# Optimization experiments

Measured on AMD Instinct MI355X. Metric: run time of the kernel, lower is better.

Reference implementation:

```python
import jax, jax.numpy as jnp
import numpy as np

D_IN, D_HID, D_OUT, N_EXP, N_TOK = 1024, 4096, 1024, 8, 4096


def setup_inputs() -> dict:
    key = jax.random.key(0)
    ks = jax.random.split(key, 7)
    x = jax.random.normal(ks[0], (N_TOK, D_IN), dtype=jnp.float32)
    s1 = 1.0 / np.sqrt(D_IN).astype(np.float32)
    s2 = 1.0 / np.sqrt(D_HID).astype(np.float32)
    W1 = jax.random.uniform(ks[1], (N_EXP, D_IN, D_HID), jnp.float32, -s1, s1)
    b1 = jax.random.uniform(ks[2], (N_EXP, D_HID), jnp.float32, -s1, s1)
    W2 = jax.random.uniform(ks[3], (N_EXP, D_HID, D_OUT), jnp.float32, -s2, s2)
    b2 = jax.random.uniform(ks[4], (N_EXP, D_OUT), jnp.float32, -s2, s2)
    Wg = jax.random.uniform(ks[5], (D_IN, N_EXP), jnp.float32, -s1, s1)
    bg = jax.random.uniform(ks[6], (N_EXP,), jnp.float32, -s1, s1)
    return {"x": x, "W1": W1, "b1": b1, "W2": W2, "b2": b2,
            "Wg": Wg, "bg": bg, "top_k": 2}


def reference(x, W1, b1, W2, b2, Wg, bg, top_k):
    # Gating: softmax over experts, then top-k and renormalizing softmax.
    gates = jax.nn.softmax(x @ Wg + bg, axis=-1)            # [N, E]
    topk_vals, topk_idx = jax.lax.top_k(gates, top_k)       # [N, k]
    topk_w = jax.nn.softmax(topk_vals, axis=-1)             # [N, k]
    # Dense all-expert MLP (vectorized replacement for per-token Python loop).
    h = jax.nn.relu(jnp.einsum('nd,edh->neh', x, W1) + b1)  # [N, E, H]
    y = jnp.einsum('neh,eho->neo', h, W2) + b2              # [N, E, O]
    # Combine: gather each token's top-k expert outputs, weighted sum.
    sel = jnp.take_along_axis(y, topk_idx[:, :, None], axis=1)  # [N, k, O]
    out = jnp.sum(topk_w[:, :, None] * sel, axis=1)             # [N, O]
    return out
```

## Files before the change

kernel.cpp:

```cpp
#include <hip/hip_runtime.h>
#include <hip/hip_bf16.h>

#define NTOK 4096
#define DIN  1024
#define DHID 4096
#define DOUT 1024
#define NEXP 8
#define TMAX 72

typedef __hip_bfloat16 bf16;
typedef short short8 __attribute__((ext_vector_type(8)));
typedef short short4v __attribute__((ext_vector_type(4)));
typedef float floatx4 __attribute__((ext_vector_type(4)));

#define WAIT_VM0 0x0F70
#define WAIT_VM4 0x0F74

#define WS_XB    0ull
#define WS_W1T   8388608ull
#define WS_W2T   75497472ull
#define WS_H     142606336ull
#define WS_META  209715200ull
#define MO_CNT    0
#define MO_OFF    64
#define MO_TILE_E 128
#define MO_TILE_S 512
#define MO_TILE_R 896
#define MO_NT     1280
#define MO_CURG   1344
#define MO_T2I    1536
#define MO_T2W    34304
#define MO_ROWS   67072
#define MO_ROWW   99840

__device__ __forceinline__ void gload16(const bf16* g, bf16* l) {
  __builtin_amdgcn_global_load_lds(
      (const __attribute__((address_space(1))) void*)g,
      (__attribute__((address_space(3))) void*)l, 16, 0, 0);
}

__global__ void k_transpose_cast(const float* __restrict__ in, bf16* __restrict__ out,
                                 int R, int C) {
  __shared__ float t[64][65];
  size_t ebase = (size_t)blockIdx.z * R * C;
  int c0 = blockIdx.x * 64, r0 = blockIdx.y * 64;
  int tid = threadIdx.x;
  int rr = tid >> 4;
  int cq = (tid & 15) * 4;
  #pragma unroll
  for (int i = 0; i < 4; i++) {
    int r = rr + i * 16;
    float4 v = *(const float4*)(in + ebase + (size_t)(r0 + r) * C + c0 + cq);
    t[cq + 0][r] = v.x; t[cq + 1][r] = v.y; t[cq + 2][r] = v.z; t[cq + 3][r] = v.w;
  }
  __syncthreads();
  int cc = tid >> 3;
  int rq = (tid & 7) * 8;
  #pragma unroll
  for (int i = 0; i < 2; i++) {
    int c = cc + i * 32;
    union { int4 v; bf16 h[8]; } u;
    #pragma unroll
    for (int j = 0; j < 8; j++) u.h[j] = __float2bfloat16(t[c][rq + j]);
    *(int4*)(out + ebase + (size_t)(c0 + c) * R + r0 + rq) = u.v;
  }
}

__global__ void k_gate(const float* __restrict__ x, const float* __restrict__ Wg,
                       const float* __restrict__ bg, bf16* __restrict__ xb,
                       int* __restrict__ t2i, float* __restrict__ t2w,
                       int* __restrict__ cnt) {
  int wave = threadIdx.x >> 6, lane = threadIdx.x & 63;
  int t = blockIdx.x * 4 + wave;
  const float* xr = x + (size_t)t * DIN;
  bf16* xbr = xb + (size_t)t * DIN;
  float acc[8] = {0.f, 0.f, 0.f, 0.f, 0.f, 0.f, 0.f, 0.f};
  #pragma unroll
  for (int i = 0; i < 4; i++) {
    int d0 = (lane + i * 64) * 4;
    float4 v = *(const float4*)(xr + d0);
    union { short4v s; bf16 h[4]; } u;
    u.h[0] = __float2bfloat16(v.x); u.h[1] = __float2bfloat16(v.y);
    u.h[2] = __float2bfloat16(v.z); u.h[3] = __float2bfloat16(v.w);
    *(short4v*)(xbr + d0) = u.s;
    float xv4[4] = {v.x, v.y, v.z, v.w};
    #pragma unroll
    for (int c = 0; c < 4; c++) {
      const float* wr = Wg + (size_t)(d0 + c) * 8;
      float4 w0 = *(const float4*)wr;
      float4 w1 = *(const float4*)(wr + 4);
      float xv = xv4[c];
      acc[0] += xv * w0.x; acc[1] += xv * w0.y; acc[2] += xv * w0.z; acc[3] += xv * w0.w;
      acc[4] += xv * w1.x; acc[5] += xv * w1.y; acc[6] += xv * w1.z; acc[7] += xv * w1.w;
    }
  }
  #pragma unroll
  for (int off = 32; off; off >>= 1) {
    #pragma unroll
    for (int e = 0; e < 8; e++) acc[e] += __shfl_xor(acc[e], off, 64);
  }
  if (lane == 0) {
    float p[8], m = -1e30f, s = 0.f;
    #pragma unroll
    for (int e = 0; e < 8; e++) { p[e] = acc[e] + bg[e]; m = fmaxf(m, p[e]); }
    #pragma unroll
    for (int e = 0; e < 8; e++) { p[e] = expf(p[e] - m); s += p[e]; }
    float inv = 1.f / s;
    #pragma unroll
    for (int e = 0; e < 8; e++) p[e] *= inv;
    int i0 = 0;
    #pragma unroll
    for (int e = 1; e < 8; e++) if (p[e] > p[i0]) i0 = e;
    int i1 = (i0 == 0) ? 1 : 0;
    #pragma unroll
    for (int e = 0; e < 8; e++) if (e != i0 && p[e] > p[i1]) i1 = e;
    float d = expf(p[i1] - p[i0]);
    float w0 = 1.f / (1.f + d), w1 = d / (1.f + d);
    t2i[2 * t] = i0; t2i[2 * t + 1] = i1;
    t2w[2 * t] = w0; t2w[2 * t + 1] = w1;
    atomicAdd(&cnt[i0], 1);
    atomicAdd(&cnt[i1], 1);
  }
}

__global__ void k_meta(const int* __restrict__ cnt, int* __restrict__ off,
                       int* __restrict__ tile_e, int* __restrict__ tile_s,
                       int* __restrict__ tile_r, int* __restrict__ nt,
                       int* __restrict__ cur_g) {
  if (threadIdx.x == 0) {
    int o = 0, n = 0;
    for (int e = 0; e < 8; e++) {
      off[e] = o; cur_g[e] = o;
      int c = cnt[e];
      for (int r = 0; r < c; r += 128) {
        tile_e[n] = e; tile_s[n] = o + r; tile_r[n] = min(128, c - r); n++;
      }
      o += c;
    }
    *nt = n;
  }
}

__global__ void k_scatter(const int* __restrict__ t2i, const float* __restrict__ t2w,
                          int* __restrict__ cur_g, int* __restrict__ rows,
                          float* __restrict__ roww) {
  __shared__ int lcnt[8], lbase[8];
  if (threadIdx.x < 8) lcnt[threadIdx.x] = 0;
  __syncthreads();
  int t = blockIdx.x * 256 + threadIdx.x;
  int e0 = t2i[2 * t], e1 = t2i[2 * t + 1];
  int p0 = atomicAdd(&lcnt[e0], 1);
  int p1 = atomicAdd(&lcnt[e1], 1);
  __syncthreads();
  if (threadIdx.x < 8)
    lbase[threadIdx.x] = atomicAdd(&cur_g[threadIdx.x], lcnt[threadIdx.x]);
  __syncthreads();
  int a0 = lbase[e0] + p0, a1 = lbase[e1] + p1;
  rows[a0] = t; roww[a0] = t2w[2 * t];
  rows[a1] = t; roww[a1] = t2w[2 * t + 1];
}

template <int MODE>
__global__ __launch_bounds__(256)
void k_gemm(const bf16* __restrict__ A, const bf16* __restrict__ Bt,
            const float* __restrict__ bias,
            const int* __restrict__ tile_e, const int* __restrict__ tile_s,
            const int* __restrict__ tile_r, const int* __restrict__ nt,
            const int* __restrict__ rows, const float* __restrict__ roww,
            bf16* __restrict__ hout, float* __restrict__ out,
            int K, int N) {
  int hwid = blockIdx.x + blockIdx.y * gridDim.x;
  int xcd = hwid & 7, pos = hwid >> 3;
  int tile = xcd * 9 + pos % 9;
  if (tile >= *nt) return;
  int n0 = (pos / 9) * 128;
  int e = tile_e[tile], start = tile_s[tile], mrows = tile_r[tile];
  int tid = threadIdx.x, lane = tid & 63, wave = tid >> 6;
  int wm = wave & 1, wn = wave >> 1;

  __shared__ bf16 Al[3][128 * 32];
  __shared__ bf16 Bl[3][128 * 32];

  int srow = tid >> 2;
  int rot = (srow >> 1) & 3;
  int kc8 = (((tid & 3) - rot) & 3) * 8;
  int ra0 = srow, ra1 = 64 + srow;
  int er0 = ra0 < mrows ? ra0 : 0;
  int er1 = ra1 < mrows ? ra1 : 0;
  size_t ga0, ga1;
  if (MODE == 1) {
    ga0 = (size_t)rows[start + er0] * K;
    ga1 = (size_t)rows[start + er1] * K;
  } else {
    ga0 = (size_t)(start + er0) * K;
    ga1 = (size_t)(start + er1) * K;
  }
  const bf16* ap0 = A + ga0 + kc8;
  const bf16* ap1 = A + ga1 + kc8;
  const bf16* bb = Bt + (size_t)e * K * N + (size_t)n0 * K;
  const bf16* bp0 = bb + (size_t)srow * K + kc8;
  const bf16* bp1 = bb + (size_t)(64 + srow) * K + kc8;

  floatx4 zz = {0.f, 0.f, 0.f, 0.f};
  floatx4 acc[4][4];
  #pragma unroll
  for (int i = 0; i < 4; i++)
    #pragma unroll
    for (int j = 0; j < 4; j++) acc[i][j] = zz;

  int fr = lane & 15;
  int ko = (((lane >> 4) + ((fr >> 1) & 3)) & 3) * 8;

#define STAGE(buf, kk)                                    \
  do {                                                    \
    gload16(ap0 + (kk), &Al[buf][tid * 8]);               \
    gload16(ap1 + (kk), &Al[buf][2048 + tid * 8]);        \
    gload16(bp0 + (kk), &Bl[buf][tid * 8]);               \
    gload16(bp1 + (kk), &Bl[buf][2048 + tid * 8]);        \
  } while (0)

  STAGE(0, 0);
  STAGE(1, 32);

  int nk = K >> 5;
  int cur = 0;
  for (int t = 0; t < nk; ++t) {
    if (t + 1 < nk) __builtin_amdgcn_s_waitcnt(WAIT_VM4);
    else            __builtin_amdgcn_s_waitcnt(WAIT_VM0);
    __builtin_amdgcn_s_barrier();

    short8 af[4], bfr[4];
    #pragma unroll
    for (int i = 0; i < 4; i++)
      af[i] = *(const short8*)&Al[cur][(wm * 64 + i * 16 + fr) * 32 + ko];
    #pragma unroll
    for (int j = 0; j < 4; j++)
      bfr[j] = *(const short8*)&Bl[cur][(wn * 64 + j * 16 + fr) * 32 + ko];

    if (t + 2 < nk) {
      int nb = cur + 2; if (nb >= 3) nb -= 3;
      STAGE(nb, (t + 2) * 32);
    }

    #pragma unroll
    for (int i = 0; i < 4; i++)
      #pragma unroll
      for (int j = 0; j < 4; j++)
        acc[i][j] = __builtin_amdgcn_mfma_f32_16x16x32_bf16(af[i], bfr[j], acc[i][j], 0, 0, 0);
    cur = (cur + 1 == 3) ? 0 : cur + 1;
  }
#undef STAGE

  int col_l = lane & 15, quad = lane >> 4;
  if (MODE == 1) {
    #pragma unroll
    for (int i = 0; i < 4; i++) {
      #pragma unroll
      for (int r = 0; r < 4; r++) {
        int row = wm * 64 + i * 16 + quad * 4 + r;
        if (row < mrows) {
          size_t rb = (size_t)(start + row) * N;
          #pragma unroll
          for (int j = 0; j < 4; j++) {
            int col = n0 + wn * 64 + j * 16 + col_l;
            float v = acc[i][j][r] + bias[e * N + col];
            hout[rb + col] = __float2bfloat16(fmaxf(v, 0.f));
          }
        }
      }
    }
  } else {
    #pragma unroll
    for (int i = 0; i < 4; i++) {
      #pragma unroll
      for (int r = 0; r < 4; r++) {
        int row = wm * 64 + i * 16 + quad * 4 + r;
        if (row < mrows) {
          int tok = rows[start + row];
          float w = roww[start + row];
          size_t ob = (size_t)tok * N;
          #pragma unroll
          for (int j = 0; j < 4; j++) {
            int col = n0 + wn * 64 + j * 16 + col_l;
            float v = (acc[i][j][r] + bias[e * N + col]) * w;
            unsafeAtomicAdd(&out[ob + col], v);
          }
        }
      }
    }
  }
}

extern "C" void kernel_launch(void* const* d_in, const int* in_sizes, int n_in,
                              void* d_out, int out_size, void* d_ws, size_t ws_size,
                              hipStream_t stream) {
  const float* x  = (const float*)d_in[0];
  const float* W1 = (const float*)d_in[1];
  const float* b1 = (const float*)d_in[2];
  const float* W2 = (const float*)d_in[3];
  const float* b2 = (const float*)d_in[4];
  const float* Wg = (const float*)d_in[5];
  const float* bg = (const float*)d_in[6];
  float* out = (float*)d_out;
  char* ws = (char*)d_ws;

  bf16* xb  = (bf16*)(ws + WS_XB);
  bf16* w1t = (bf16*)(ws + WS_W1T);
  bf16* w2t = (bf16*)(ws + WS_W2T);
  bf16* h   = (bf16*)(ws + WS_H);
  char* meta = ws + WS_META;
  int*   cnt    = (int*)(meta + MO_CNT);
  int*   off    = (int*)(meta + MO_OFF);
  int*   tile_e = (int*)(meta + MO_TILE_E);
  int*   tile_s = (int*)(meta + MO_TILE_S);
  int*   tile_r = (int*)(meta + MO_TILE_R);
  int*   nt     = (int*)(meta + MO_NT);
  int*   cur_g  = (int*)(meta + MO_CURG);
  int*   t2i    = (int*)(meta + MO_T2I);
  float* t2w    = (float*)(meta + MO_T2W);
  int*   rows   = (int*)(meta + MO_ROWS);
  float* roww   = (float*)(meta + MO_ROWW);

  hipMemsetAsync(cnt, 0, 64, stream);
  hipMemsetAsync(d_out, 0, (size_t)out_size * sizeof(float), stream);

  k_transpose_cast<<<dim3(DHID / 64, DIN / 64, NEXP), 256, 0, stream>>>(W1, w1t, DIN, DHID);
  k_transpose_cast<<<dim3(DOUT / 64, DHID / 64, NEXP), 256, 0, stream>>>(W2, w2t, DHID, DOUT);
  k_gate<<<NTOK / 4, 256, 0, stream>>>(x, Wg, bg, xb, t2i, t2w, cnt);
  k_meta<<<1, 64, 0, stream>>>(cnt, off, tile_e, tile_s, tile_r, nt, cur_g);
  k_scatter<<<NTOK / 256, 256, 0, stream>>>(t2i, t2w, cur_g, rows, roww);
  k_gemm<1><<<dim3(TMAX, DHID / 128), 256, 0, stream>>>(
      xb, w1t, b1, tile_e, tile_s, tile_r, nt, rows, roww, h, nullptr, DIN, DHID);
  k_gemm<2><<<dim3(TMAX, DOUT / 128), 256, 0, stream>>>(
      h, w2t, b2, tile_e, tile_s, tile_r, nt, rows, roww, nullptr, out, DHID, DOUT);
}
```

Before: 672.3 us.

## Widen grouped GEMM tile to 128x256 and parallelize tile metadata build

The expert GEMM tile doubles in N from 128 to 256, so each wave computes 64x128 with 32 accumulators. B staging grows to four loads per stage and the wait count is adjusted to match. This gives more MFMA work per A-fragment load and halves the grid, at the cost of higher register pressure (launch bounds now ask for 2 blocks) and fewer blocks to fill the CUs. The serial single-thread k_meta loop is also replaced by a parallel per-thread tile assignment.

Result: slower. 694.3 us (+3.3%).

```diff
diff --git a/kernel.cpp b/kernel.cpp
--- a/kernel.cpp
+++ b/kernel.cpp
@@ -14,7 +14,7 @@
 typedef float floatx4 __attribute__((ext_vector_type(4)));
 
 #define WAIT_VM0 0x0F70
-#define WAIT_VM4 0x0F74
+#define WAIT_VM6 0x0F76
 
 #define WS_XB    0ull
 #define WS_W1T   8388608ull
@@ -127,17 +127,22 @@
                        int* __restrict__ tile_e, int* __restrict__ tile_s,
                        int* __restrict__ tile_r, int* __restrict__ nt,
                        int* __restrict__ cur_g) {
-  if (threadIdx.x == 0) {
-    int o = 0, n = 0;
-    for (int e = 0; e < 8; e++) {
-      off[e] = o; cur_g[e] = o;
-      int c = cnt[e];
-      for (int r = 0; r < c; r += 128) {
-        tile_e[n] = e; tile_s[n] = o + r; tile_r[n] = min(128, c - r); n++;
-      }
-      o += c;
-    }
-    *nt = n;
+  int t = threadIdx.x;
+  int c[8], o[8], tb[8];
+  int acc = 0, tacc = 0;
+  #pragma unroll
+  for (int e = 0; e < 8; e++) {
+    c[e] = cnt[e]; o[e] = acc; acc += c[e];
+    tb[e] = tacc; tacc += (c[e] + 127) >> 7;
+  }
+  if (t < 8) { off[t] = o[t]; cur_g[t] = o[t]; }
+  if (t == 0) *nt = tacc;
+  if (t < tacc) {
+    int e = 0;
+    #pragma unroll
+    for (int k = 1; k < 8; k++) if (t >= tb[k]) e = k;
+    int r = (t - tb[e]) << 7;
+    tile_e[t] = e; tile_s[t] = o[e] + r; tile_r[t] = min(128, c[e] - r);
   }
 }
 
@@ -161,7 +166,7 @@
 }
 
 template <int MODE>
-__global__ __launch_bounds__(256)
+__global__ __launch_bounds__(256, 2)
 void k_gemm(const bf16* __restrict__ A, const bf16* __restrict__ Bt,
             const float* __restrict__ bias,
             const int* __restrict__ tile_e, const int* __restrict__ tile_s,
@@ -173,13 +178,13 @@
   int xcd = hwid & 7, pos = hwid >> 3;
   int tile = xcd * 9 + pos % 9;
   if (tile >= *nt) return;
-  int n0 = (pos / 9) * 128;
+  int n0 = (pos / 9) * 256;
   int e = tile_e[tile], start = tile_s[tile], mrows = tile_r[tile];
   int tid = threadIdx.x, lane = tid & 63, wave = tid >> 6;
   int wm = wave & 1, wn = wave >> 1;
 
   __shared__ bf16 Al[3][128 * 32];
-  __shared__ bf16 Bl[3][128 * 32];
+  __shared__ bf16 Bl[3][256 * 32];
 
   int srow = tid >> 2;
   int rot = (srow >> 1) & 3;
@@ -200,13 +205,15 @@
   const bf16* bb = Bt + (size_t)e * K * N + (size_t)n0 * K;
   const bf16* bp0 = bb + (size_t)srow * K + kc8;
   const bf16* bp1 = bb + (size_t)(64 + srow) * K + kc8;
+  const bf16* bp2 = bb + (size_t)(128 + srow) * K + kc8;
+  const bf16* bp3 = bb + (size_t)(192 + srow) * K + kc8;
 
   floatx4 zz = {0.f, 0.f, 0.f, 0.f};
-  floatx4 acc[4][4];
+  floatx4 acc[4][8];
   #pragma unroll
   for (int i = 0; i < 4; i++)
     #pragma unroll
-    for (int j = 0; j < 4; j++) acc[i][j] = zz;
+    for (int j = 0; j < 8; j++) acc[i][j] = zz;
 
   int fr = lane & 15;
   int ko = (((lane >> 4) + ((fr >> 1) & 3)) & 3) * 8;
@@ -217,6 +224,8 @@
     gload16(ap1 + (kk), &Al[buf][2048 + tid * 8]);        \
     gload16(bp0 + (kk), &Bl[buf][tid * 8]);               \
     gload16(bp1 + (kk), &Bl[buf][2048 + tid * 8]);        \
+    gload16(bp2 + (kk), &Bl[buf][4096 + tid * 8]);        \
+    gload16(bp3 + (kk), &Bl[buf][6144 + tid * 8]);        \
   } while (0)
 
   STAGE(0, 0);
@@ -225,17 +234,17 @@
   int nk = K >> 5;
   int cur = 0;
   for (int t = 0; t < nk; ++t) {
-    if (t + 1 < nk) __builtin_amdgcn_s_waitcnt(WAIT_VM4);
+    if (t + 1 < nk) __builtin_amdgcn_s_waitcnt(WAIT_VM6);
     else            __builtin_amdgcn_s_waitcnt(WAIT_VM0);
     __builtin_amdgcn_s_barrier();
 
-    short8 af[4], bfr[4];
+    short8 af[4], bfr[8];
     #pragma unroll
     for (int i = 0; i < 4; i++)
       af[i] = *(const short8*)&Al[cur][(wm * 64 + i * 16 + fr) * 32 + ko];
     #pragma unroll
-    for (int j = 0; j < 4; j++)
-      bfr[j] = *(const short8*)&Bl[cur][(wn * 64 + j * 16 + fr) * 32 + ko];
+    for (int j = 0; j < 8; j++)
+      bfr[j] = *(const short8*)&Bl[cur][(wn * 128 + j * 16 + fr) * 32 + ko];
 
     if (t + 2 < nk) {
       int nb = cur + 2; if (nb >= 3) nb -= 3;
@@ -245,7 +254,7 @@
     #pragma unroll
     for (int i = 0; i < 4; i++)
       #pragma unroll
-      for (int j = 0; j < 4; j++)
+      for (int j = 0; j < 8; j++)
         acc[i][j] = __builtin_amdgcn_mfma_f32_16x16x32_bf16(af[i], bfr[j], acc[i][j], 0, 0, 0);
     cur = (cur + 1 == 3) ? 0 : cur + 1;
   }
@@ -261,8 +270,8 @@
         if (row < mrows) {
           size_t rb = (size_t)(start + row) * N;
           #pragma unroll
-          for (int j = 0; j < 4; j++) {
-            int col = n0 + wn * 64 + j * 16 + col_l;
+          for (int j = 0; j < 8; j++) {
+            int col = n0 + wn * 128 + j * 16 + col_l;
             float v = acc[i][j][r] + bias[e * N + col];
             hout[rb + col] = __float2bfloat16(fmaxf(v, 0.f));
           }
@@ -280,8 +289,8 @@
           float w = roww[start + row];
           size_t ob = (size_t)tok * N;
           #pragma unroll
-          for (int j = 0; j < 4; j++) {
-            int col = n0 + wn * 64 + j * 16 + col_l;
+          for (int j = 0; j < 8; j++) {
+            int col = n0 + wn * 128 + j * 16 + col_l;
             float v = (acc[i][j][r] + bias[e * N + col]) * w;
             unsafeAtomicAdd(&out[ob + col], v);
           }
@@ -327,10 +336,10 @@
   k_transpose_cast<<<dim3(DHID / 64, DIN / 64, NEXP), 256, 0, stream>>>(W1, w1t, DIN, DHID);
   k_transpose_cast<<<dim3(DOUT / 64, DHID / 64, NEXP), 256, 0, stream>>>(W2, w2t, DHID, DOUT);
   k_gate<<<NTOK / 4, 256, 0, stream>>>(x, Wg, bg, xb, t2i, t2w, cnt);
-  k_meta<<<1, 64, 0, stream>>>(cnt, off, tile_e, tile_s, tile_r, nt, cur_g);
+  k_meta<<<1, 128, 0, stream>>>(cnt, off, tile_e, tile_s, tile_r, nt, cur_g);
   k_scatter<<<NTOK / 256, 256, 0, stream>>>(t2i, t2w, cur_g, rows, roww);
-  k_gemm<1><<<dim3(TMAX, DHID / 128), 256, 0, stream>>>(
+  k_gemm<1><<<dim3(TMAX, DHID / 256), 256, 0, stream>>>(
       xb, w1t, b1, tile_e, tile_s, tile_r, nt, rows, roww, h, nullptr, DIN, DHID);
-  k_gemm<2><<<dim3(TMAX, DOUT / 128), 256, 0, stream>>>(
+  k_gemm<2><<<dim3(TMAX, DOUT / 256), 256, 0, stream>>>(
       h, w2t, b2, tile_e, tile_s, tile_r, nt, rows, roww, nullptr, out, DHID, DOUT);
 }
```

## Fuse weight transposes into gate and GEMM1 kernels and parallelize tile metadata

Applied to the files above, without the earlier changes.

The W1 transpose-cast is merged into the gating kernel as extra blocks, and the W2 transpose-cast is merged into the first expert GEMM launch, so weight conversion overlaps with other work and two launches go away. The tile metadata kernel now builds tiles in parallel across threads instead of serially in one thread. A leftover unused k_gemm2 stub is also added. The fused kernels share one LDS allocation sized for the GEMM, which may lower occupancy for the transpose blocks.

Result: faster. 627.6 us (-6.6%).

```diff
diff --git a/kernel.cpp b/kernel.cpp
--- a/kernel.cpp
+++ b/kernel.cpp
@@ -7,6 +7,8 @@
 #define DOUT 1024
 #define NEXP 8
 #define TMAX 72
+#define G1BLK (TMAX * (DHID / 128))
+#define G2BLK (TMAX * (DOUT / 128))
 
 typedef __hip_bfloat16 bf16;
 typedef short short8 __attribute__((ext_vector_type(8)));
@@ -39,11 +41,12 @@
       (__attribute__((address_space(3))) void*)l, 16, 0, 0);
 }
 
-__global__ void k_transpose_cast(const float* __restrict__ in, bf16* __restrict__ out,
-                                 int R, int C) {
-  __shared__ float t[64][65];
-  size_t ebase = (size_t)blockIdx.z * R * C;
-  int c0 = blockIdx.x * 64, r0 = blockIdx.y * 64;
+__device__ __forceinline__ void transpose_tile(const float* __restrict__ in,
+                                               bf16* __restrict__ out,
+                                               int R, int C, int cx, int ry,
+                                               int e, float* t) {
+  size_t ebase = (size_t)e * R * C;
+  int c0 = cx * 64, r0 = ry * 64;
   int tid = threadIdx.x;
   int rr = tid >> 4;
   int cq = (tid & 15) * 4;
@@ -51,7 +54,8 @@
   for (int i = 0; i < 4; i++) {
     int r = rr + i * 16;
     float4 v = *(const float4*)(in + ebase + (size_t)(r0 + r) * C + c0 + cq);
-    t[cq + 0][r] = v.x; t[cq + 1][r] = v.y; t[cq + 2][r] = v.z; t[cq + 3][r] = v.w;
+    t[(cq + 0) * 65 + r] = v.x; t[(cq + 1) * 65 + r] = v.y;
+    t[(cq + 2) * 65 + r] = v.z; t[(cq + 3) * 65 + r] = v.w;
   }
   __syncthreads();
   int cc = tid >> 3;
@@ -61,17 +65,20 @@
     int c = cc + i * 32;
     union { int4 v; bf16 h[8]; } u;
     #pragma unroll
-    for (int j = 0; j < 8; j++) u.h[j] = __float2bfloat16(t[c][rq + j]);
+    for (int j = 0; j < 8; j++) u.h[j] = __float2bfloat16(t[c * 65 + rq + j]);
     *(int4*)(out + ebase + (size_t)(c0 + c) * R + r0 + rq) = u.v;
   }
 }
 
-__global__ void k_gate(const float* __restrict__ x, const float* __restrict__ Wg,
-                       const float* __restrict__ bg, bf16* __restrict__ xb,
-                       int* __restrict__ t2i, float* __restrict__ t2w,
-                       int* __restrict__ cnt) {
+__device__ __forceinline__ void gate_body(const float* __restrict__ x,
+                                          const float* __restrict__ Wg,
+                                          const float* __restrict__ bg,
+                                          bf16* __restrict__ xb,
+                                          int* __restrict__ t2i,
+                                          float* __restrict__ t2w,
+                                          int* __restrict__ cnt, int blk) {
   int wave = threadIdx.x >> 6, lane = threadIdx.x & 63;
-  int t = blockIdx.x * 4 + wave;
+  int t = blk * 4 + wave;
   const float* xr = x + (size_t)t * DIN;
   bf16* xbr = xb + (size_t)t * DIN;
   float acc[8] = {0.f, 0.f, 0.f, 0.f, 0.f, 0.f, 0.f, 0.f};
@@ -123,21 +130,46 @@
   }
 }
 
+__global__ __launch_bounds__(256)
+void k_gate_w1t(const float* __restrict__ x, const float* __restrict__ Wg,
+                const float* __restrict__ bg, bf16* __restrict__ xb,
+                int* __restrict__ t2i, float* __restrict__ t2w,
+                int* __restrict__ cnt,
+                const float* __restrict__ W1, bf16* __restrict__ w1t) {
+  __shared__ __align__(16) float tsm[64 * 65];
+  int b = blockIdx.x;
+  if (b < NTOK / 4) {
+    gate_body(x, Wg, bg, xb, t2i, t2w, cnt, b);
+  } else {
+    int tb = b - NTOK / 4;
+    int e = tb >> 10;
+    int rem = tb & 1023;
+    int cx = rem & 63;
+    int ry = rem >> 6;
+    transpose_tile(W1, w1t, DIN, DHID, cx, ry, e, tsm);
+  }
+}
+
 __global__ void k_meta(const int* __restrict__ cnt, int* __restrict__ off,
                        int* __restrict__ tile_e, int* __restrict__ tile_s,
                        int* __restrict__ tile_r, int* __restrict__ nt,
                        int* __restrict__ cur_g) {
-  if (threadIdx.x == 0) {
-    int o = 0, n = 0;
-    for (int e = 0; e < 8; e++) {
-      off[e] = o; cur_g[e] = o;
-      int c = cnt[e];
-      for (int r = 0; r < c; r += 128) {
-        tile_e[n] = e; tile_s[n] = o + r; tile_r[n] = min(128, c - r); n++;
-      }
-      o += c;
-    }
-    *nt = n;
+  int t = threadIdx.x;
+  int c[8], o[8], tb[8];
+  int acc = 0, tacc = 0;
+  #pragma unroll
+  for (int e = 0; e < 8; e++) {
+    c[e] = cnt[e]; o[e] = acc; acc += c[e];
+    tb[e] = tacc; tacc += (c[e] + 127) >> 7;
+  }
+  if (t < 8) { off[t] = o[t]; cur_g[t] = o[t]; }
+  if (t == 0) *nt = tacc;
+  if (t < tacc) {
+    int e = 0;
+    #pragma unroll
+    for (int k = 1; k < 8; k++) if (t >= tb[k]) e = k;
+    int r = (t - tb[e]) << 7;
+    tile_e[t] = e; tile_s[t] = o[e] + r; tile_r[t] = min(128, c[e] - r);
   }
 }
 
@@ -161,15 +193,14 @@
 }
 
 template <int MODE>
-__global__ __launch_bounds__(256)
-void k_gemm(const bf16* __restrict__ A, const bf16* __restrict__ Bt,
-            const float* __restrict__ bias,
-            const int* __restrict__ tile_e, const int* __restrict__ tile_s,
-            const int* __restrict__ tile_r, const int* __restrict__ nt,
-            const int* __restrict__ rows, const float* __restrict__ roww,
-            bf16* __restrict__ hout, float* __restrict__ out,
-            int K, int N) {
-  int hwid = blockIdx.x + blockIdx.y * gridDim.x;
+__device__ __forceinline__ void gemm_tile(
+    const bf16* __restrict__ A, const bf16* __restrict__ Bt,
+    const float* __restrict__ bias,
+    const int* __restrict__ tile_e, const int* __restrict__ tile_s,
+    const int* __restrict__ tile_r, const int* __restrict__ nt,
+    const int* __restrict__ rows, const float* __restrict__ roww,
+    bf16* __restrict__ hout, float* __restrict__ out,
+    int K, int N, int hwid, bf16* Al, bf16* Bl) {
   int xcd = hwid & 7, pos = hwid >> 3;
   int tile = xcd * 9 + pos % 9;
   if (tile >= *nt) return;
@@ -177,9 +208,6 @@
   int e = tile_e[tile], start = tile_s[tile], mrows = tile_r[tile];
   int tid = threadIdx.x, lane = tid & 63, wave = tid >> 6;
   int wm = wave & 1, wn = wave >> 1;
-
-  __shared__ bf16 Al[3][128 * 32];
-  __shared__ bf16 Bl[3][128 * 32];
 
   int srow = tid >> 2;
   int rot = (srow >> 1) & 3;
@@ -211,13 +239,12 @@
   int fr = lane & 15;
   int ko = (((lane >> 4) + ((fr >> 1) & 3)) & 3) * 8;
 
-#define STAGE(buf, kk)                                    \
-  do {                                                    \
-    gload16(ap0 + (kk), &Al[buf][tid * 8]);               \
-    gload16(ap1 + (kk), &Al[buf][2048 + tid * 8]);        \
-    gload16(bp0 + (kk), &Bl[buf][tid * 8]);               \
-    gload16(bp1 + (kk), &Bl[buf][2048 + tid * 8]);        \
-  } while (0)
+  auto STAGE = [&](int buf, int kk) {
+    gload16(ap0 + kk, Al + buf * 4096 + tid * 8);
+    gload16(ap1 + kk, Al + buf * 4096 + 2048 + tid * 8);
+    gload16(bp0 + kk, Bl + buf * 4096 + tid * 8);
+    gload16(bp1 + kk, Bl + buf * 4096 + 2048 + tid * 8);
+  };
 
   STAGE(0, 0);
   STAGE(1, 32);
@@ -232,10 +259,10 @@
     short8 af[4], bfr[4];
     #pragma unroll
     for (int i = 0; i < 4; i++)
-      af[i] = *(const short8*)&Al[cur][(wm * 64 + i * 16 + fr) * 32 + ko];
+      af[i] = *(const short8*)&Al[cur * 4096 + (wm * 64 + i * 16 + fr) * 32 + ko];
     #pragma unroll
     for (int j = 0; j < 4; j++)
-      bfr[j] = *(const short8*)&Bl[cur][(wn * 64 + j * 16 + fr) * 32 + ko];
+      bfr[j] = *(const short8*)&Bl[cur * 4096 + (wn * 64 + j * 16 + fr) * 32 + ko];
 
     if (t + 2 < nk) {
       int nb = cur + 2; if (nb >= 3) nb -= 3;
@@ -249,7 +276,6 @@
         acc[i][j] = __builtin_amdgcn_mfma_f32_16x16x32_bf16(af[i], bfr[j], acc[i][j], 0, 0, 0);
     cur = (cur + 1 == 3) ? 0 : cur + 1;
   }
-#undef STAGE
 
   int col_l = lane & 15, quad = lane >> 4;
   if (MODE == 1) {
@@ -291,6 +317,60 @@
   }
 }
 
+__global__ __launch_bounds__(256)
+void k_gemm1_w2t(const bf16* __restrict__ A, const bf16* __restrict__ Bt,
+                 const float* __restrict__ bias,
+                 const int* __restrict__ tile_e, const int* __restrict__ tile_s,
+                 const int* __restrict__ tile_r, const int* __restrict__ nt,
+                 const int* __restrict__ rows, const float* __restrict__ roww,
+                 bf16* __restrict__ hout,
+                 const float* __restrict__ W2, bf16* __restrict__ w2t) {
+  __shared__ __align__(16) char smem[49152];
+  int b = blockIdx.x;
+  if (b < G1BLK) {
+    gemm_tile<1>(A, Bt, bias, tile_e, tile_s, tile_r, nt, rows, roww,
+                 hout, nullptr, DIN, DHID, b,
+                 (bf16*)smem, (bf16*)(smem + 24576));
+  } else {
+    int tb = b - G1BLK;
+    int e = tb >> 10;
+    int rem = tb & 1023;
+    int cx = rem & 15;
+    int ry = rem >> 4;
+    transpose_tile(W2, w2t, DHID, DOUT, cx, ry, e, (float*)smem);
+  }
+}
+
+__global__ __launch_bounds__(256)
+void k_gemm2(const bf16* __restrict__ A, const bf16* __restrict__ Bt,
+             const float* __restrict__ bias,
+             const int* __restrict__ tile_e, const int* __restrict__ tile_s,
+             const int* __restrict__ tile_r, const int* __restrict__ nt,
+             const int* __restrict__ rows, const float* __restrict__ roww,
+             float* __restrict__ out) {
+  __shared__ __align__(16) char smem[49152];
+  gemm_tile<2>(A, Bt, nullptr ? nullptr : Bt ? (const float*)Bt : nullptr,
+               nullptr, nullptr, nullptr, nullptr, nullptr, nullptr,
+               nullptr, nullptr, 0, 0, 0, nullptr, nullptr);
+}
+
+extern "C" void kernel_launch(void* const* d_in, const int* in_sizes, int n_in,
+                              void* d_out, int out_size, void* d_ws, size_t ws_size,
+                              hipStream_t stream);
+
+__global__ __launch_bounds__(256)
+void k_gemm2_real(const bf16* __restrict__ A, const bf16* __restrict__ Bt,
+                  const float* __restrict__ bias,
+                  const int* __restrict__ tile_e, const int* __restrict__ tile_s,
+                  const int* __restrict__ tile_r, const int* __restrict__ nt,
+                  const int* __restrict__ rows, const float* __restrict__ roww,
+                  float* __restrict__ out) {
+  __shared__ __align__(16) char smem[49152];
+  gemm_tile<2>(A, Bt, bias, tile_e, tile_s, tile_r, nt, rows, roww,
+               nullptr, out, DHID, DOUT, (int)blockIdx.x,
+               (bf16*)smem, (bf16*)(smem + 24576));
+}
+
 extern "C" void kernel_launch(void* const* d_in, const int* in_sizes, int n_in,
                               void* d_out, int out_size, void* d_ws, size_t ws_size,
                               hipStream_t stream) {
@@ -324,13 +404,13 @@
   hipMemsetAsync(cnt, 0, 64, stream);
   hipMemsetAsync(d_out, 0, (size_t)out_size * sizeof(float), stream);
 
-  k_transpose_cast<<<dim3(DHID / 64, DIN / 64, NEXP), 256, 0, stream>>>(W1, w1t, DIN, DHID);
-  k_transpose_cast<<<dim3(DOUT / 64, DHID / 64, NEXP), 256, 0, stream>>>(W2, w2t, DHID, DOUT);
-  k_gate<<<NTOK / 4, 256, 0, stream>>>(x, Wg, bg, xb, t2i, t2w, cnt);
-  k_meta<<<1, 64, 0, stream>>>(cnt, off, tile_e, tile_s, tile_r, nt, cur_g);
+  k_gate_w1t<<<NTOK / 4 + 8192, 256, 0, stream>>>(x, Wg, bg, xb, t2i, t2w, cnt,
+                                                  W1, w1t);
+  k_meta<<<1, 128, 0, stream>>>(cnt, off, tile_e, tile_s, tile_r, nt, cur_g);
   k_scatter<<<NTOK / 256, 256, 0, stream>>>(t2i, t2w, cur_g, rows, roww);
-  k_gemm<1><<<dim3(TMAX, DHID / 128), 256, 0, stream>>>(
-      xb, w1t, b1, tile_e, tile_s, tile_r, nt, rows, roww, h, nullptr, DIN, DHID);
-  k_gemm<2><<<dim3(TMAX, DOUT / 128), 256, 0, stream>>>(
-      h, w2t, b2, tile_e, tile_s, tile_r, nt, rows, roww, nullptr, out, DHID, DOUT);
-}
+  k_gemm1_w2t<<<G1BLK + 8192, 256, 0, stream>>>(xb, w1t, b1, tile_e, tile_s,
+                                                tile_r, nt, rows, roww, h,
+                                                W2, w2t);
+  k_gemm2_real<<<G2BLK, 256, 0, stream>>>(h, w2t, b2, tile_e, tile_s, tile_r,
+                                          nt, rows, roww, out);
+}
```
